# Kernel tuning notes

Measured on AMD Instinct MI355X. Metric: run time of the kernel, lower is better.

Reference implementation:

```python
import jax, jax.numpy as jnp
import numpy as np
import math

B, L, H, NH = 8, 512, 512, 8
DH = H // NH


def setup_inputs() -> dict:
    key = jax.random.key(0)
    ks = jax.random.split(key, 12)
    src = jax.random.normal(ks[0], (B, L, H), dtype=jnp.float32)
    seq_len = jax.random.randint(ks[1], (B,), L // 2, L + 1).astype(jnp.int32)
    seq_len = seq_len.at[0].set(L)  # guarantee max(seq_len) == L
    pe = jax.random.normal(ks[2], (2 * L, H), dtype=jnp.float32) * 0.02
    s = 1.0 / math.sqrt(H)
    Wq = jax.random.normal(ks[3], (H, H), dtype=jnp.float32) * s
    bq = jnp.zeros((H,), jnp.float32)
    Wk = jax.random.normal(ks[4], (H, H), dtype=jnp.float32) * s
    bk = jnp.zeros((H,), jnp.float32)
    Wv = jax.random.normal(ks[5], (H, H), dtype=jnp.float32) * s
    bv = jnp.zeros((H,), jnp.float32)
    Wr = jax.random.normal(ks[6], (H, H), dtype=jnp.float32) * s
    br = jnp.zeros((H,), jnp.float32)
    u = jax.random.normal(ks[7], (NH, DH), dtype=jnp.float32) * 0.02
    v = jax.random.normal(ks[8], (NH, DH), dtype=jnp.float32) * 0.02
    gamma = jnp.ones((H,), jnp.float32)
    beta = jnp.zeros((H,), jnp.float32)
    return dict(src=src, seq_len=seq_len, pe=pe, Wq=Wq, bq=bq, Wk=Wk, bk=bk,
                Wv=Wv, bv=bv, Wr=Wr, br=br, u=u, v=v, gamma=gamma, beta=beta)


def reference(src, seq_len, pe, Wq, bq, Wk, bk, Wv, bv, Wr, br, u, v, gamma, beta):
    b, l, h = src.shape
    dh = h // NH
    # relative distance rel[i,j] = j - i, lookup pe[rel + L]  -> [L, L, H]
    rel = jnp.arange(l)[None, :] - jnp.arange(l)[:, None]
    R = pe[rel + l]
    # projections (torch Linear: y = x W^T + b)
    q = src @ Wq.T + bq
    k = src @ Wk.T + bk
    val = src @ Wv.T + bv
    R = R @ Wr.T + br
    # split heads
    q = q.reshape(b, l, NH, dh)
    k = k.reshape(b, l, NH, dh)
    val = val.reshape(b, l, NH, dh)
    R = R.reshape(l, l, NH, dh)
    # Transformer-XL score terms
    A = jnp.einsum('bihd,bjhd->bhij', q, k)
    Bt = jnp.einsum('bihd,ijhd->bhij', q, R)
    C = jnp.einsum('hd,bjhd->bhj', u, k)[:, :, None, :]
    D = jnp.einsum('ijhd,hd->hij', R, v)[None]
    scores = (A + Bt + C + D) / math.sqrt(dh)
    # key-side padding mask
    mask = jnp.arange(l)[None, :] < seq_len[:, None]  # [B, L]
    scores = jnp.where(mask[:, None, None, :], scores, jnp.float32(-1e15))
    attn = jax.nn.softmax(scores, axis=-1)
    out = jnp.einsum('bhij,bjhd->bihd', attn, val).reshape(b, l, h)
    res = src + out
    # LayerNorm (eps=1e-5) then exact GELU
    mu = jnp.mean(res, axis=-1, keepdims=True)
    var = jnp.mean((res - mu) ** 2, axis=-1, keepdims=True)
    ln = (res - mu) * jax.lax.rsqrt(var + 1e-5) * gamma + beta
    return jax.nn.gelu(ln, approximate=False)
```

## Files before the change

### kernel.cpp

```cpp
#include <hip/hip_runtime.h>
#include <math.h>

#define Bn 8
#define Ln 512
#define Hn 512
#define NHn 8
#define DHn 64

typedef __attribute__((ext_vector_type(8))) short short8;
typedef __attribute__((ext_vector_type(4))) float f32x4;

__device__ __forceinline__ unsigned short f2bf(float f) {
    unsigned int u = __float_as_uint(f);
    unsigned int r = (u + 0x7FFFu + ((u >> 16) & 1u)) >> 16;
    return (unsigned short)r;
}
__device__ __forceinline__ float bf2f(unsigned short s) {
    return __uint_as_float(((unsigned int)s) << 16);
}

__device__ __forceinline__ void gload_lds16(const void* g, void* l) {
    __builtin_amdgcn_global_load_lds(
        (const __attribute__((address_space(1))) unsigned int*)g,
        (__attribute__((address_space(3))) unsigned int*)l,
        16, 0, 0);
}

__global__ __launch_bounds__(256) void convert_kernel(
    const float* __restrict__ src, const float* __restrict__ pe,
    const float* __restrict__ Wq, const float* __restrict__ Wk,
    const float* __restrict__ Wv, const float* __restrict__ Wr,
    const float* __restrict__ bq, const float* __restrict__ bk,
    const float* __restrict__ bv,
    unsigned short* __restrict__ src_bf, unsigned short* __restrict__ pe_bf,
    unsigned short* __restrict__ Wcat_bf, unsigned short* __restrict__ Wr_bf,
    float* __restrict__ bcat)
{
    const int bid = blockIdx.x;
    const int tid = threadIdx.x;
    const float* in; unsigned short* outp; int base4;
    if (bid < 2048)      { in = src; outp = src_bf;           base4 = bid; }
    else if (bid < 2560) { in = pe;  outp = pe_bf;            base4 = bid - 2048; }
    else if (bid < 2816) { in = Wq;  outp = Wcat_bf;          base4 = bid - 2560; }
    else if (bid < 3072) { in = Wk;  outp = Wcat_bf + 262144; base4 = bid - 2816; }
    else if (bid < 3328) { in = Wv;  outp = Wcat_bf + 524288; base4 = bid - 3072; }
    else if (bid < 3584) { in = Wr;  outp = Wr_bf;            base4 = bid - 3328; }
    else {
        const int idx = (bid - 3584) * 256 + tid;
        if (idx < 512)            bcat[idx] = bq[idx];
        else if (idx < 1024)      bcat[idx] = bk[idx - 512];
        else if (idx < 1536)      bcat[idx] = bv[idx - 1024];
        return;
    }
    const int i4 = (base4 * 256 + tid) * 4;
    float4 x = *(const float4*)&in[i4];
    ushort4 o;
    o.x = f2bf(x.x); o.y = f2bf(x.y); o.z = f2bf(x.z); o.w = f2bf(x.w);
    *(ushort4*)&outp[i4] = o;
}

__global__ __launch_bounds__(256) void mfma_nt_kernel(
    const unsigned short* __restrict__ src_bf,
    const unsigned short* __restrict__ Wcat_bf,
    const float* __restrict__ bcat,
    unsigned short* __restrict__ QKb,
    unsigned short* __restrict__ VTg,
    const unsigned short* __restrict__ pe_bf,
    const unsigned short* __restrict__ Wr_bf,
    const float* __restrict__ br,
    unsigned short* __restrict__ Rpb)
{
    const unsigned short* A; const unsigned short* B;
    int m0, n0, mode;
    if (blockIdx.z == 0) {
        if (blockIdx.x < 8) {
            mode = 0; A = src_bf;  m0 = blockIdx.y * 128;
            B = Wcat_bf; n0 = blockIdx.x * 128;
        } else {
            mode = 1; A = Wcat_bf; m0 = blockIdx.x * 128;
            B = src_bf;  n0 = blockIdx.y * 128;
        }
    } else {
        if (blockIdx.x >= 4 || blockIdx.y >= 8) return;
        mode = 2; A = pe_bf; m0 = blockIdx.y * 128;
        B = Wr_bf; n0 = blockIdx.x * 128;
    }

    __shared__ unsigned short As[128 * 32];
    __shared__ unsigned short Bs[128 * 32];

    const int t = threadIdx.x;
    const int wave = t >> 6, lane = t & 63;
    const int wm = (wave >> 1) * 64;
    const int wn = (wave & 1) * 64;

    f32x4 acc[4][4] = {};

    const int srow = wave * 32 + (lane >> 2);
    const int scol = (lane & 3) * 8;
    const unsigned short* Ag = A + (size_t)(m0 + srow) * 512 + scol;
    const unsigned short* Bg = B + (size_t)(n0 + srow) * 512 + scol;
    unsigned short* AsW = &As[srow * 32 + scol];
    unsigned short* BsW = &Bs[srow * 32 + scol];

    for (int k0 = 0; k0 < 512; k0 += 32) {
        __syncthreads();
        gload_lds16(Ag + k0,            AsW);
        gload_lds16(Ag + k0 + 16 * 512, AsW + 16 * 32);
        gload_lds16(Bg + k0,            BsW);
        gload_lds16(Bg + k0 + 16 * 512, BsW + 16 * 32);
        __syncthreads();

        short8 af[4], bf[4];
        #pragma unroll
        for (int mt = 0; mt < 4; ++mt)
            af[mt] = *(const short8*)&As[(wm + mt * 16 + (lane & 15)) * 32 + (lane >> 4) * 8];
        #pragma unroll
        for (int nt = 0; nt < 4; ++nt)
            bf[nt] = *(const short8*)&Bs[(wn + nt * 16 + (lane & 15)) * 32 + (lane >> 4) * 8];
        #pragma unroll
        for (int mt = 0; mt < 4; ++mt)
            #pragma unroll
            for (int nt = 0; nt < 4; ++nt)
                acc[mt][nt] = __builtin_amdgcn_mfma_f32_16x16x32_bf16(
                    af[mt], bf[nt], acc[mt][nt], 0, 0, 0);
    }

    const int crow = (lane >> 4) * 4;
    const int ccol = lane & 15;
    if (mode == 0) {
        #pragma unroll
        for (int mt = 0; mt < 4; ++mt)
            #pragma unroll
            for (int nt = 0; nt < 4; ++nt) {
                const int n = n0 + wn + nt * 16 + ccol;
                const float bn = bcat[n];
                #pragma unroll
                for (int r = 0; r < 4; ++r) {
                    const int m = m0 + wm + mt * 16 + crow + r;
                    QKb[(size_t)m * 1024 + n] = f2bf(acc[mt][nt][r] + bn);
                }
            }
    } else if (mode == 1) {
        #pragma unroll
        for (int mt = 0; mt < 4; ++mt)
            #pragma unroll
            for (int nt = 0; nt < 4; ++nt) {
                const int n = n0 + wn + nt * 16 + ccol;
                #pragma unroll
                for (int r = 0; r < 4; ++r) {
                    const int m = m0 + wm + mt * 16 + crow + r;
                    VTg[(size_t)(m - 1024) * 4096 + n] = f2bf(acc[mt][nt][r] + bcat[m]);
                }
            }
    } else {
        #pragma unroll
        for (int mt = 0; mt < 4; ++mt)
            #pragma unroll
            for (int nt = 0; nt < 4; ++nt) {
                const int n = n0 + wn + nt * 16 + ccol;
                const float bn = br[n];
                #pragma unroll
                for (int r = 0; r < 4; ++r) {
                    const int m = m0 + wm + mt * 16 + crow + r;
                    Rpb[(size_t)m * 512 + n] = f2bf(acc[mt][nt][r] + bn);
                }
            }
    }
}

#define PADK 72
#define QRS 133
__global__ __launch_bounds__(256) void attn_kernel(
    const unsigned short* __restrict__ QKb,
    const unsigned short* __restrict__ VTg,
    const unsigned short* __restrict__ Rpb,
    const float* __restrict__ u, const float* __restrict__ v,
    const int* __restrict__ seq_len, float* __restrict__ O)
{
    const int i0 = blockIdx.x * 64;
    const int h  = blockIdx.y;
    const int b  = blockIdx.z;
    const int slen = seq_len[b];

    __shared__ unsigned short k_s [64 * PADK];
    __shared__ unsigned short vT_s[64 * PADK];
    __shared__ unsigned short rs_s[64 * PADK];
    __shared__ unsigned short p_s [64 * PADK];
    __shared__ unsigned short qrT [64 * QRS];

    const int t = threadIdx.x;
    const int wave = t >> 6, lane = t & 63;
    const int l = lane & 15, g = lane >> 4;

    short8 af_qu[2], af_qv[2];
    {
        const unsigned short* qrow =
            QKb + (size_t)(b * 512 + i0 + wave * 16 + l) * 1024 + h * 64;
        #pragma unroll
        for (int kk = 0; kk < 2; ++kk) {
            const int c = kk * 32 + g * 8;
            unsigned short q8[8];
            *(uint4*)q8 = *(const uint4*)(qrow + c);
            float4 u0 = *(const float4*)(u + h * 64 + c);
            float4 u1 = *(const float4*)(u + h * 64 + c + 4);
            float4 v0 = *(const float4*)(v + h * 64 + c);
            float4 v1 = *(const float4*)(v + h * 64 + c + 4);
            float uf[8] = {u0.x,u0.y,u0.z,u0.w,u1.x,u1.y,u1.z,u1.w};
            float vf[8] = {v0.x,v0.y,v0.z,v0.w,v1.x,v1.y,v1.z,v1.w};
            short8 qu, qv;
            #pragma unroll
            for (int e = 0; e < 8; ++e) {
                float qf = bf2f(q8[e]);
                qu[e] = (short)f2bf(qf + uf[e]);
                qv[e] = (short)f2bf(qf + vf[e]);
            }
            af_qu[kk] = qu; af_qv[kk] = qv;
        }
    }

    float m_run[4], l_run[4];
    f32x4 accO[4] = {};
    #pragma unroll
    for (int r = 0; r < 4; ++r) { m_run[r] = -3.0e38f; l_run[r] = 0.f; }

    const int jr = t >> 2, c0 = (t & 3) * 16;

    for (int jt = 0; jt < 8; ++jt) {
        const int j0 = jt * 64;
        __syncthreads();

        {
            const unsigned short* kp =
                QKb + (size_t)(b * 512 + j0 + jr) * 1024 + 512 + h * 64 + c0;
            *(uint4*)(k_s + jr * PADK + c0)     = *(const uint4*)(kp);
            *(uint4*)(k_s + jr * PADK + c0 + 8) = *(const uint4*)(kp + 8);
            const unsigned short* vp =
                VTg + (size_t)(h * 64 + jr) * 4096 + b * 512 + j0 + c0;
            *(uint4*)(vT_s + jr * PADK + c0)     = *(const uint4*)(vp);
            *(uint4*)(vT_s + jr * PADK + c0 + 8) = *(const uint4*)(vp + 8);
        }

        const int nchunk = (jt == 0) ? 2 : 1;
        for (int c = 0; c < nchunk; ++c) {
            const int g_base = (jt == 0) ? (448 - i0 + 64 * c) : (j0 - i0 + 512);
            {
                const unsigned short* rp =
                    Rpb + (size_t)(g_base + jr) * 512 + h * 64 + c0;
                *(uint4*)(rs_s + jr * PADK + c0)     = *(const uint4*)(rp);
                *(uint4*)(rs_s + jr * PADK + c0 + 8) = *(const uint4*)(rp + 8);
            }
            __syncthreads();
            const int slot0 = (g_base & 127);
            #pragma unroll
            for (int nt8 = 0; nt8 < 4; ++nt8) {
                f32x4 a = {};
                #pragma unroll
                for (int kk = 0; kk < 2; ++kk) {
                    short8 br8 = *(const short8*)&rs_s[(nt8 * 16 + l) * PADK + kk * 32 + g * 8];
                    a = __builtin_amdgcn_mfma_f32_16x16x32_bf16(af_qv[kk], br8, a, 0, 0, 0);
                }
                const int sl = slot0 + nt8 * 16 + l;
                #pragma unroll
                for (int r = 0; r < 4; ++r)
                    qrT[(wave * 16 + g * 4 + r) * QRS + sl] = f2bf(a[r]);
            }
            if (c + 1 < nchunk) __syncthreads();
        }
        __syncthreads();

        f32x4 accA[4];
        #pragma unroll
        for (int nt = 0; nt < 4; ++nt) {
            f32x4 a = {};
            #pragma unroll
            for (int kk = 0; kk < 2; ++kk) {
                short8 bk = *(const short8*)&k_s[(nt * 16 + l) * PADK + kk * 32 + g * 8];
                a = __builtin_amdgcn_mfma_f32_16x16x32_bf16(af_qu[kk], bk, a, 0, 0, 0);
            }
            accA[nt] = a;
        }

        float sv[4][4];
        #pragma unroll
        for (int nt = 0; nt < 4; ++nt)
            #pragma unroll
            for (int r = 0; r < 4; ++r) {
                const int il = wave * 16 + g * 4 + r;
                const int slot = (j0 + nt * 16 + l - i0 - il + 512) & 127;
                const float qr = bf2f(qrT[il * QRS + slot]);
                float s = (accA[nt][r] + qr) * 0.125f;
                if (j0 + nt * 16 + l >= slen) s = -1e15f;
                sv[nt][r] = s;
            }

        float alpha_r[4];
        #pragma unroll
        for (int r = 0; r < 4; ++r) {
            float tm = fmaxf(fmaxf(sv[0][r], sv[1][r]), fmaxf(sv[2][r], sv[3][r]));
            tm = fmaxf(tm, __shfl_xor(tm, 1, 64));
            tm = fmaxf(tm, __shfl_xor(tm, 2, 64));
            tm = fmaxf(tm, __shfl_xor(tm, 4, 64));
            tm = fmaxf(tm, __shfl_xor(tm, 8, 64));
            const float mn = fmaxf(m_run[r], tm);
            alpha_r[r] = __expf(m_run[r] - mn);
            m_run[r] = mn;
            float ss = 0.f;
            #pragma unroll
            for (int nt = 0; nt < 4; ++nt) {
                const float p = __expf(sv[nt][r] - mn);
                sv[nt][r] = p; ss += p;
            }
            ss += __shfl_xor(ss, 1, 64);
            ss += __shfl_xor(ss, 2, 64);
            ss += __shfl_xor(ss, 4, 64);
            ss += __shfl_xor(ss, 8, 64);
            l_run[r] = l_run[r] * alpha_r[r] + ss;
        }

        #pragma unroll
        for (int nt = 0; nt < 4; ++nt)
            #pragma unroll
            for (int r = 0; r < 4; ++r)
                p_s[(wave * 16 + g * 4 + r) * PADK + nt * 16 + l] = f2bf(sv[nt][r]);
        __builtin_amdgcn_sched_barrier(0);

        #pragma unroll
        for (int nt = 0; nt < 4; ++nt)
            #pragma unroll
            for (int r = 0; r < 4; ++r)
                accO[nt][r] *= alpha_r[r];

        short8 pa[2];
        #pragma unroll
        for (int kk = 0; kk < 2; ++kk)
            pa[kk] = *(const short8*)&p_s[(wave * 16 + l) * PADK + kk * 32 + g * 8];
        #pragma unroll
        for (int nt = 0; nt < 4; ++nt) {
            #pragma unroll
            for (int kk = 0; kk < 2; ++kk) {
                short8 bv8 = *(const short8*)&vT_s[(nt * 16 + l) * PADK + kk * 32 + g * 8];
                accO[nt] = __builtin_amdgcn_mfma_f32_16x16x32_bf16(pa[kk], bv8, accO[nt], 0, 0, 0);
            }
        }
    }

    float inv[4];
    #pragma unroll
    for (int r = 0; r < 4; ++r) inv[r] = 1.0f / l_run[r];
    #pragma unroll
    for (int nt = 0; nt < 4; ++nt)
        #pragma unroll
        for (int r = 0; r < 4; ++r)
            O[(size_t)(b * 512 + i0 + wave * 16 + g * 4 + r) * 512 + h * 64 + nt * 16 + l]
                = accO[nt][r] * inv[r];
}

__global__ __launch_bounds__(256) void ln_gelu_kernel(
    const float* __restrict__ src, const float* __restrict__ O,
    const float* __restrict__ gamma, const float* __restrict__ beta,
    float* __restrict__ out)
{
    const int row  = blockIdx.x * 4 + (threadIdx.x >> 6);
    const int lane = threadIdx.x & 63;
    const float* s = &src[(size_t)row * 512];
    const float* o = &O[(size_t)row * 512];
    float x[8];
    float sum = 0.f;
    #pragma unroll
    for (int e = 0; e < 8; ++e) {
        x[e] = s[lane + e * 64] + o[lane + e * 64];
        sum += x[e];
    }
    #pragma unroll
    for (int off = 32; off >= 1; off >>= 1) sum += __shfl_xor(sum, off, 64);
    const float mean = sum * (1.0f / 512.0f);
    float var = 0.f;
    #pragma unroll
    for (int e = 0; e < 8; ++e) { float d = x[e] - mean; var += d * d; }
    #pragma unroll
    for (int off = 32; off >= 1; off >>= 1) var += __shfl_xor(var, off, 64);
    var *= (1.0f / 512.0f);
    const float inv = rsqrtf(var + 1e-5f);
    #pragma unroll
    for (int e = 0; e < 8; ++e) {
        const int c = lane + e * 64;
        float ln = (x[e] - mean) * inv * gamma[c] + beta[c];
        out[(size_t)row * 512 + c] = 0.5f * ln * (1.0f + erff(ln * 0.70710678118654752f));
    }
}

extern "C" void kernel_launch(void* const* d_in, const int* in_sizes, int n_in,
                              void* d_out, int out_size, void* d_ws, size_t ws_size,
                              hipStream_t stream)
{
    const float* src     = (const float*)d_in[0];
    const int*   seq_len = (const int*)  d_in[1];
    const float* pe      = (const float*)d_in[2];
    const float* Wq      = (const float*)d_in[3];
    const float* bq      = (const float*)d_in[4];
    const float* Wk      = (const float*)d_in[5];
    const float* bk      = (const float*)d_in[6];
    const float* Wv      = (const float*)d_in[7];
    const float* bv      = (const float*)d_in[8];
    const float* Wr      = (const float*)d_in[9];
    const float* br      = (const float*)d_in[10];
    const float* u       = (const float*)d_in[11];
    const float* v       = (const float*)d_in[12];
    const float* gamma   = (const float*)d_in[13];
    const float* beta    = (const float*)d_in[14];
    float* out = (float*)d_out;

    char* w = (char*)d_ws;
    unsigned short* QKb     = (unsigned short*)(w);
    unsigned short* VTg     = (unsigned short*)(w + 8388608);
    unsigned short* Rpb     = (unsigned short*)(w + 12582912);
    float*          O       = (float*)         (w + 13631488);
    unsigned short* src_bf  = (unsigned short*)(w + 22020096);
    unsigned short* pe_bf   = (unsigned short*)(w + 26214400);
    unsigned short* Wcat_bf = (unsigned short*)(w + 27262976);
    unsigned short* Wr_bf   = (unsigned short*)(w + 28835840);
    float*          bcat    = (float*)         (w + 29360128);

    convert_kernel<<<dim3(3590), 256, 0, stream>>>(
        src, pe, Wq, Wk, Wv, Wr, bq, bk, bv,
        src_bf, pe_bf, Wcat_bf, Wr_bf, bcat);

    mfma_nt_kernel<<<dim3(12, 32, 2), 256, 0, stream>>>(
        src_bf, Wcat_bf, bcat, QKb, VTg,
        pe_bf, Wr_bf, br, Rpb);

    attn_kernel<<<dim3(8, NHn, Bn), 256, 0, stream>>>(QKb, VTg, Rpb, u, v, seq_len, O);

    ln_gelu_kernel<<<dim3(Bn * Ln / 4), 256, 0, stream>>>(src, O, gamma, beta, out);
}
```

Baseline: 142.1 us.

## Fuse fp32-to-bf16 conversion into projection GEMM and store attention output as bf16

Result: no change. 144.5 us (+1.7%).

```diff
diff --git a/kernel.cpp b/kernel.cpp
--- a/kernel.cpp
+++ b/kernel.cpp
@@ -18,72 +18,38 @@
 __device__ __forceinline__ float bf2f(unsigned short s) {
     return __uint_as_float(((unsigned int)s) << 16);
 }
-
-__device__ __forceinline__ void gload_lds16(const void* g, void* l) {
-    __builtin_amdgcn_global_load_lds(
-        (const __attribute__((address_space(1))) unsigned int*)g,
-        (__attribute__((address_space(3))) unsigned int*)l,
-        16, 0, 0);
-}
-
-__global__ __launch_bounds__(256) void convert_kernel(
+__device__ __forceinline__ uint2 pack4(float4 v) {
+    uint2 r;
+    r.x = (unsigned)f2bf(v.x) | ((unsigned)f2bf(v.y) << 16);
+    r.y = (unsigned)f2bf(v.z) | ((unsigned)f2bf(v.w) << 16);
+    return r;
+}
+
+__global__ __launch_bounds__(256) void gemm_kernel(
     const float* __restrict__ src, const float* __restrict__ pe,
     const float* __restrict__ Wq, const float* __restrict__ Wk,
     const float* __restrict__ Wv, const float* __restrict__ Wr,
     const float* __restrict__ bq, const float* __restrict__ bk,
-    const float* __restrict__ bv,
-    unsigned short* __restrict__ src_bf, unsigned short* __restrict__ pe_bf,
-    unsigned short* __restrict__ Wcat_bf, unsigned short* __restrict__ Wr_bf,
-    float* __restrict__ bcat)
+    const float* __restrict__ bv, const float* __restrict__ br,
+    unsigned short* __restrict__ QKb,
+    unsigned short* __restrict__ VTg,
+    unsigned short* __restrict__ Rpb)
 {
     const int bid = blockIdx.x;
-    const int tid = threadIdx.x;
-    const float* in; unsigned short* outp; int base4;
-    if (bid < 2048)      { in = src; outp = src_bf;           base4 = bid; }
-    else if (bid < 2560) { in = pe;  outp = pe_bf;            base4 = bid - 2048; }
-    else if (bid < 2816) { in = Wq;  outp = Wcat_bf;          base4 = bid - 2560; }
-    else if (bid < 3072) { in = Wk;  outp = Wcat_bf + 262144; base4 = bid - 2816; }
-    else if (bid < 3328) { in = Wv;  outp = Wcat_bf + 524288; base4 = bid - 3072; }
-    else if (bid < 3584) { in = Wr;  outp = Wr_bf;            base4 = bid - 3328; }
-    else {
-        const int idx = (bid - 3584) * 256 + tid;
-        if (idx < 512)            bcat[idx] = bq[idx];
-        else if (idx < 1024)      bcat[idx] = bk[idx - 512];
-        else if (idx < 1536)      bcat[idx] = bv[idx - 1024];
-        return;
-    }
-    const int i4 = (base4 * 256 + tid) * 4;
-    float4 x = *(const float4*)&in[i4];
-    ushort4 o;
-    o.x = f2bf(x.x); o.y = f2bf(x.y); o.z = f2bf(x.z); o.w = f2bf(x.w);
-    *(ushort4*)&outp[i4] = o;
-}
-
-__global__ __launch_bounds__(256) void mfma_nt_kernel(
-    const unsigned short* __restrict__ src_bf,
-    const unsigned short* __restrict__ Wcat_bf,
-    const float* __restrict__ bcat,
-    unsigned short* __restrict__ QKb,
-    unsigned short* __restrict__ VTg,
-    const unsigned short* __restrict__ pe_bf,
-    const unsigned short* __restrict__ Wr_bf,
-    const float* __restrict__ br,
-    unsigned short* __restrict__ Rpb)
-{
-    const unsigned short* A; const unsigned short* B;
-    int m0, n0, mode;
-    if (blockIdx.z == 0) {
-        if (blockIdx.x < 8) {
-            mode = 0; A = src_bf;  m0 = blockIdx.y * 128;
-            B = Wcat_bf; n0 = blockIdx.x * 128;
-        } else {
-            mode = 1; A = Wcat_bf; m0 = blockIdx.x * 128;
-            B = src_bf;  n0 = blockIdx.y * 128;
-        }
+    int mode, m0, n0;
+    const float *Ab, *Bb;
+    if (bid < 256) {
+        mode = 0; n0 = (bid & 7) * 128; m0 = (bid >> 3) * 128;
+        Ab = src + (size_t)m0 * 512;
+        Bb = (n0 < 512) ? (Wq + (size_t)n0 * 512) : (Wk + (size_t)(n0 - 512) * 512);
+    } else if (bid < 384) {
+        mode = 1; m0 = ((bid - 256) & 3) * 128; n0 = ((bid - 256) >> 2) * 128;
+        Ab = Wv + (size_t)m0 * 512;
+        Bb = src + (size_t)n0 * 512;
     } else {
-        if (blockIdx.x >= 4 || blockIdx.y >= 8) return;
-        mode = 2; A = pe_bf; m0 = blockIdx.y * 128;
-        B = Wr_bf; n0 = blockIdx.x * 128;
+        mode = 2; n0 = ((bid - 384) & 3) * 128; m0 = ((bid - 384) >> 2) * 128;
+        Ab = pe + (size_t)m0 * 512;
+        Bb = Wr + (size_t)n0 * 512;
     }
 
     __shared__ unsigned short As[128 * 32];
@@ -94,21 +60,31 @@
     const int wm = (wave >> 1) * 64;
     const int wn = (wave & 1) * 64;
 
+    const int trow = t >> 1;
+    const int tcol = (t & 1) * 16;
+    const float* Ap = Ab + (size_t)trow * 512 + tcol;
+    const float* Bp = Bb + (size_t)trow * 512 + tcol;
+    unsigned short* AsW = &As[trow * 32 + tcol];
+    unsigned short* BsW = &Bs[trow * 32 + tcol];
+
     f32x4 acc[4][4] = {};
 
-    const int srow = wave * 32 + (lane >> 2);
-    const int scol = (lane & 3) * 8;
-    const unsigned short* Ag = A + (size_t)(m0 + srow) * 512 + scol;
-    const unsigned short* Bg = B + (size_t)(n0 + srow) * 512 + scol;
-    unsigned short* AsW = &As[srow * 32 + scol];
-    unsigned short* BsW = &Bs[srow * 32 + scol];
-
     for (int k0 = 0; k0 < 512; k0 += 32) {
+        float4 a4[4], b4[4];
+        #pragma unroll
+        for (int e = 0; e < 4; ++e) {
+            a4[e] = *(const float4*)(Ap + k0 + e * 4);
+            b4[e] = *(const float4*)(Bp + k0 + e * 4);
+        }
         __syncthreads();
-        gload_lds16(Ag + k0,            AsW);
-        gload_lds16(Ag + k0 + 16 * 512, AsW + 16 * 32);
-        gload_lds16(Bg + k0,            BsW);
-        gload_lds16(Bg + k0 + 16 * 512, BsW + 16 * 32);
+        {
+            uint2 p0 = pack4(a4[0]), p1 = pack4(a4[1]), p2 = pack4(a4[2]), p3 = pack4(a4[3]);
+            *(uint4*)(AsW)     = make_uint4(p0.x, p0.y, p1.x, p1.y);
+            *(uint4*)(AsW + 8) = make_uint4(p2.x, p2.y, p3.x, p3.y);
+            uint2 q0 = pack4(b4[0]), q1 = pack4(b4[1]), q2 = pack4(b4[2]), q3 = pack4(b4[3]);
+            *(uint4*)(BsW)     = make_uint4(q0.x, q0.y, q1.x, q1.y);
+            *(uint4*)(BsW + 8) = make_uint4(q2.x, q2.y, q3.x, q3.y);
+        }
         __syncthreads();
 
         short8 af[4], bf[4];
@@ -134,7 +110,7 @@
             #pragma unroll
             for (int nt = 0; nt < 4; ++nt) {
                 const int n = n0 + wn + nt * 16 + ccol;
-                const float bn = bcat[n];
+                const float bn = (n < 512) ? bq[n] : bk[n - 512];
                 #pragma unroll
                 for (int r = 0; r < 4; ++r) {
                     const int m = m0 + wm + mt * 16 + crow + r;
@@ -149,8 +125,8 @@
                 const int n = n0 + wn + nt * 16 + ccol;
                 #pragma unroll
                 for (int r = 0; r < 4; ++r) {
-                    const int m = m0 + wm + mt * 16 + crow + r;
-                    VTg[(size_t)(m - 1024) * 4096 + n] = f2bf(acc[mt][nt][r] + bcat[m]);
+                    const int dv = m0 + wm + mt * 16 + crow + r;
+                    VTg[(size_t)dv * 4096 + n] = f2bf(acc[mt][nt][r] + bv[dv]);
                 }
             }
     } else {
@@ -176,7 +152,7 @@
     const unsigned short* __restrict__ VTg,
     const unsigned short* __restrict__ Rpb,
     const float* __restrict__ u, const float* __restrict__ v,
-    const int* __restrict__ seq_len, float* __restrict__ O)
+    const int* __restrict__ seq_len, unsigned short* __restrict__ Ob)
 {
     const int i0 = blockIdx.x * 64;
     const int h  = blockIdx.y;
@@ -267,7 +243,6 @@
             }
             if (c + 1 < nchunk) __syncthreads();
         }
-        __syncthreads();
 
         f32x4 accA[4];
         #pragma unroll
@@ -275,8 +250,8 @@
             f32x4 a = {};
             #pragma unroll
             for (int kk = 0; kk < 2; ++kk) {
-                short8 bk = *(const short8*)&k_s[(nt * 16 + l) * PADK + kk * 32 + g * 8];
-                a = __builtin_amdgcn_mfma_f32_16x16x32_bf16(af_qu[kk], bk, a, 0, 0, 0);
+                short8 bk8 = *(const short8*)&k_s[(nt * 16 + l) * PADK + kk * 32 + g * 8];
+                a = __builtin_amdgcn_mfma_f32_16x16x32_bf16(af_qu[kk], bk8, a, 0, 0, 0);
             }
             accA[nt] = a;
         }
@@ -323,7 +298,6 @@
             #pragma unroll
             for (int r = 0; r < 4; ++r)
                 p_s[(wave * 16 + g * 4 + r) * PADK + nt * 16 + l] = f2bf(sv[nt][r]);
-        __builtin_amdgcn_sched_barrier(0);
 
         #pragma unroll
         for (int nt = 0; nt < 4; ++nt)
@@ -352,26 +326,31 @@
     for (int nt = 0; nt < 4; ++nt)
         #pragma unroll
         for (int r = 0; r < 4; ++r)
-            O[(size_t)(b * 512 + i0 + wave * 16 + g * 4 + r) * 512 + h * 64 + nt * 16 + l]
-                = accO[nt][r] * inv[r];
+            Ob[(size_t)(b * 512 + i0 + wave * 16 + g * 4 + r) * 512 + h * 64 + nt * 16 + l]
+                = f2bf(accO[nt][r] * inv[r]);
 }
 
 __global__ __launch_bounds__(256) void ln_gelu_kernel(
-    const float* __restrict__ src, const float* __restrict__ O,
+    const float* __restrict__ src, const unsigned short* __restrict__ Ob,
     const float* __restrict__ gamma, const float* __restrict__ beta,
     float* __restrict__ out)
 {
     const int row  = blockIdx.x * 4 + (threadIdx.x >> 6);
     const int lane = threadIdx.x & 63;
-    const float* s = &src[(size_t)row * 512];
-    const float* o = &O[(size_t)row * 512];
+    const int c0   = lane * 8;
+    const float* s = &src[(size_t)row * 512 + c0];
+    float4 s0 = *(const float4*)(s);
+    float4 s1 = *(const float4*)(s + 4);
+    unsigned short o8[8];
+    *(uint4*)o8 = *(const uint4*)(Ob + (size_t)row * 512 + c0);
     float x[8];
+    x[0] = s0.x + bf2f(o8[0]); x[1] = s0.y + bf2f(o8[1]);
+    x[2] = s0.z + bf2f(o8[2]); x[3] = s0.w + bf2f(o8[3]);
+    x[4] = s1.x + bf2f(o8[4]); x[5] = s1.y + bf2f(o8[5]);
+    x[6] = s1.z + bf2f(o8[6]); x[7] = s1.w + bf2f(o8[7]);
     float sum = 0.f;
     #pragma unroll
-    for (int e = 0; e < 8; ++e) {
-        x[e] = s[lane + e * 64] + o[lane + e * 64];
-        sum += x[e];
-    }
+    for (int e = 0; e < 8; ++e) sum += x[e];
     #pragma unroll
     for (int off = 32; off >= 1; off >>= 1) sum += __shfl_xor(sum, off, 64);
     const float mean = sum * (1.0f / 512.0f);
@@ -382,12 +361,21 @@
     for (int off = 32; off >= 1; off >>= 1) var += __shfl_xor(var, off, 64);
     var *= (1.0f / 512.0f);
     const float inv = rsqrtf(var + 1e-5f);
+    float4 g0 = *(const float4*)(gamma + c0);
+    float4 g1 = *(const float4*)(gamma + c0 + 4);
+    float4 b0 = *(const float4*)(beta + c0);
+    float4 b1 = *(const float4*)(beta + c0 + 4);
+    float gm[8] = {g0.x,g0.y,g0.z,g0.w,g1.x,g1.y,g1.z,g1.w};
+    float bt[8] = {b0.x,b0.y,b0.z,b0.w,b1.x,b1.y,b1.z,b1.w};
+    float r[8];
     #pragma unroll
     for (int e = 0; e < 8; ++e) {
-        const int c = lane + e * 64;
-        float ln = (x[e] - mean) * inv * gamma[c] + beta[c];
-        out[(size_t)row * 512 + c] = 0.5f * ln * (1.0f + erff(ln * 0.70710678118654752f));
-    }
+        float ln = (x[e] - mean) * inv * gm[e] + bt[e];
+        r[e] = 0.5f * ln * (1.0f + erff(ln * 0.70710678118654752f));
+    }
+    float* op = &out[(size_t)row * 512 + c0];
+    *(float4*)(op)     = make_float4(r[0], r[1], r[2], r[3]);
+    *(float4*)(op + 4) = make_float4(r[4], r[5], r[6], r[7]);
 }
 
 extern "C" void kernel_launch(void* const* d_in, const int* in_sizes, int n_in,
@@ -412,25 +400,15 @@
     float* out = (float*)d_out;
 
     char* w = (char*)d_ws;
-    unsigned short* QKb     = (unsigned short*)(w);
-    unsigned short* VTg     = (unsigned short*)(w + 8388608);
-    unsigned short* Rpb     = (unsigned short*)(w + 12582912);
-    float*          O       = (float*)         (w + 13631488);
-    unsigned short* src_bf  = (unsigned short*)(w + 22020096);
-    unsigned short* pe_bf   = (unsigned short*)(w + 26214400);
-    unsigned short* Wcat_bf = (unsigned short*)(w + 27262976);
-    unsigned short* Wr_bf   = (unsigned short*)(w + 28835840);
-    float*          bcat    = (float*)         (w + 29360128);
-
-    convert_kernel<<<dim3(3590), 256, 0, stream>>>(
-        src, pe, Wq, Wk, Wv, Wr, bq, bk, bv,
-        src_bf, pe_bf, Wcat_bf, Wr_bf, bcat);
-
-    mfma_nt_kernel<<<dim3(12, 32, 2), 256, 0, stream>>>(
-        src_bf, Wcat_bf, bcat, QKb, VTg,
-        pe_bf, Wr_bf, br, Rpb);
-
-    attn_kernel<<<dim3(8, NHn, Bn), 256, 0, stream>>>(QKb, VTg, Rpb, u, v, seq_len, O);
-
-    ln_gelu_kernel<<<dim3(Bn * Ln / 4), 256, 0, stream>>>(src, O, gamma, beta, out);
-}
+    unsigned short* QKb = (unsigned short*)(w);
+    unsigned short* VTg = (unsigned short*)(w + 8388608);
+    unsigned short* Rpb = (unsigned short*)(w + 12582912);
+    unsigned short* Ob  = (unsigned short*)(w + 13631488);
+
+    gemm_kernel<<<dim3(416), 256, 0, stream>>>(
+        src, pe, Wq, Wk, Wv, Wr, bq, bk, bv, br, QKb, VTg, Rpb);
+
+    attn_kernel<<<dim3(8, NHn, Bn), 256, 0, stream>>>(QKb, VTg, Rpb, u, v, seq_len, Ob);
+
+    ln_gelu_kernel<<<dim3(Bn * Ln / 4), 256, 0, stream>>>(src, Ob, gamma, beta, out);
+}
```
